# Kernel tuning notes

Hardware: AMD Instinct MI355X
Metric: run time of the kernel (lower is better)

Reference implementation:

```python
import jax, jax.numpy as jnp
import numpy as np

D_MODEL = 1024
N_HEADS = 16
D_HEAD = D_MODEL // N_HEADS


def setup_inputs() -> dict:
    key = jax.random.key(0)
    ks = jax.random.split(key, 9)
    s = 1.0 / np.sqrt(D_MODEL)
    inp = {
        'x': jax.random.normal(ks[0], (2, 2048, D_MODEL), dtype=jnp.float32),
        'wq': jax.random.uniform(ks[1], (D_MODEL, D_MODEL), jnp.float32, -s, s),
        'bq': jnp.zeros((D_MODEL,), jnp.float32),
        'wk': jax.random.uniform(ks[2], (D_MODEL, D_MODEL), jnp.float32, -s, s),
        'bk': jnp.zeros((D_MODEL,), jnp.float32),
        'wv': jax.random.uniform(ks[3], (D_MODEL, D_MODEL), jnp.float32, -s, s),
        'bv': jnp.zeros((D_MODEL,), jnp.float32),
        'wo': jax.random.uniform(ks[4], (D_MODEL, D_MODEL), jnp.float32, -s, s),
        'bo': jnp.zeros((D_MODEL,), jnp.float32),
    }
    return inp


def reference(x, wq, bq, wk, bk, wv, bv, wo, bo):
    B, S, D = x.shape
    H, Dh = N_HEADS, D_HEAD
    # projections (dropout is identity in eval mode)
    q = (x @ wq + bq).reshape(B, S, H, Dh).transpose(0, 2, 1, 3)  # [B,H,S,Dh]
    k = (x @ wk + bk).reshape(B, S, H, Dh).transpose(0, 2, 1, 3)
    v = (x @ wv + bv).reshape(B, S, H, Dh).transpose(0, 2, 1, 3)
    scores = jnp.einsum('bhqd,bhkd->bhqk', q, k) / jnp.sqrt(jnp.float32(Dh))
    causal = jnp.tril(jnp.ones((S, S), dtype=bool))  # [S,S]
    scores = jnp.where(causal[None, None], scores, jnp.float32(-jnp.inf))
    attn = jax.nn.softmax(scores, axis=-1)
    out = jnp.einsum('bhqk,bhkd->bhqd', attn, v)  # [B,H,S,Dh]
    out = out.transpose(0, 2, 1, 3).reshape(B, S, D)
    return out @ wo + bo
```

## Files before the change

kernel.cpp:

```cpp
#include <hip/hip_runtime.h>
#include <hip/hip_bf16.h>
#include <stdint.h>

#define NH 16
#define DH 64
#define BATCH 2
#define SEQ 2048
#define DMODEL 1024

typedef __attribute__((ext_vector_type(8))) short short8;
typedef __attribute__((ext_vector_type(4))) float f32x4;

#define MFMA16(a, b, c) __builtin_amdgcn_mfma_f32_16x16x32_bf16(a, b, c, 0, 0, 0)

__device__ inline unsigned short f2bf(float f) {
    union { float f; unsigned u; } v; v.f = f;
    unsigned r = v.u + 0x7fff + ((v.u >> 16) & 1);
    return (unsigned short)(r >> 16);
}

__device__ inline void gload_lds16(const unsigned short* g, unsigned short* l) {
    __builtin_amdgcn_global_load_lds((const __attribute__((address_space(1))) void*)g,
                                     (__attribute__((address_space(3))) void*)l, 16, 0, 0);
}

__device__ inline float dpp16_max(float v) {
    int t;
    t = __builtin_amdgcn_mov_dpp(__float_as_int(v), 0x121, 0xf, 0xf, false);
    v = fmaxf(v, __int_as_float(t));
    t = __builtin_amdgcn_mov_dpp(__float_as_int(v), 0x122, 0xf, 0xf, false);
    v = fmaxf(v, __int_as_float(t));
    t = __builtin_amdgcn_mov_dpp(__float_as_int(v), 0x124, 0xf, 0xf, false);
    v = fmaxf(v, __int_as_float(t));
    t = __builtin_amdgcn_mov_dpp(__float_as_int(v), 0x128, 0xf, 0xf, false);
    v = fmaxf(v, __int_as_float(t));
    return v;
}
__device__ inline float dpp16_sum(float v) {
    int t;
    t = __builtin_amdgcn_mov_dpp(__float_as_int(v), 0x121, 0xf, 0xf, false);
    v += __int_as_float(t);
    t = __builtin_amdgcn_mov_dpp(__float_as_int(v), 0x122, 0xf, 0xf, false);
    v += __int_as_float(t);
    t = __builtin_amdgcn_mov_dpp(__float_as_int(v), 0x124, 0xf, 0xf, false);
    v += __int_as_float(t);
    t = __builtin_amdgcn_mov_dpp(__float_as_int(v), 0x128, 0xf, 0xf, false);
    v += __int_as_float(t);
    return v;
}

__global__ void k_cvt(const float* __restrict__ in, unsigned short* __restrict__ out) {
    size_t i = ((size_t)blockIdx.x * 256 + threadIdx.x) * 8;
    f32x4 a = *(const f32x4*)(in + i);
    f32x4 b = *(const f32x4*)(in + i + 4);
    short8 o;
    o[0] = (short)f2bf(a[0]); o[1] = (short)f2bf(a[1]);
    o[2] = (short)f2bf(a[2]); o[3] = (short)f2bf(a[3]);
    o[4] = (short)f2bf(b[0]); o[5] = (short)f2bf(b[1]);
    o[6] = (short)f2bf(b[2]); o[7] = (short)f2bf(b[3]);
    *(short8*)(out + i) = o;
}

__global__ void k_transpose_w4(const float* __restrict__ wq, const float* __restrict__ wk,
                               const float* __restrict__ wv, const float* __restrict__ wo,
                               unsigned short* __restrict__ qkvT, unsigned short* __restrict__ oT) {
    __shared__ float tile[32][33];
    const int z = blockIdx.z;
    const float* w = (z == 0) ? wq : (z == 1) ? wk : (z == 2) ? wv : wo;
    unsigned short* out = (z == 3) ? oT : qkvT + (size_t)z * 1024 * 1024;
    int k0 = blockIdx.x * 32, n0 = blockIdx.y * 32;
    int tx = threadIdx.x, ty = threadIdx.y;
    #pragma unroll
    for (int j = 0; j < 32; j += 8)
        tile[ty + j][tx] = w[(size_t)(k0 + ty + j) * DMODEL + n0 + tx];
    __syncthreads();
    #pragma unroll
    for (int j = 0; j < 32; j += 8)
        out[(size_t)(n0 + ty + j) * DMODEL + k0 + tx] = f2bf(tile[tx][ty + j]);
}

__global__ __launch_bounds__(256) void k_transpose_v(const unsigned short* __restrict__ v,
                                                     unsigned short* __restrict__ vt) {
    __shared__ __align__(16) unsigned short tile[64][72];
    int bh = blockIdx.y, st = blockIdx.x;
    const unsigned short* src = v + ((size_t)bh * SEQ + st * 64) * DH;
    int r = threadIdx.x >> 2, c = (threadIdx.x & 3) * 16;
    *(short8*)&tile[r][c]     = *(const short8*)&src[r * DH + c];
    *(short8*)&tile[r][c + 8] = *(const short8*)&src[r * DH + c + 8];
    __syncthreads();
    int d = r, sb = c;
    short8 o0, o1;
    #pragma unroll
    for (int j = 0; j < 8; ++j) { o0[j] = (short)tile[sb + j][d]; o1[j] = (short)tile[sb + 8 + j][d]; }
    unsigned short* dst = vt + ((size_t)bh * DH + d) * SEQ + st * 64 + sb;
    *(short8*)dst = o0;
    *(short8*)(dst + 8) = o1;
}

#define GEMM_BODY(A_, Bt_)                                                              \
    __shared__ __align__(16) unsigned short As[128 * 32];                               \
    __shared__ __align__(16) unsigned short Bs[128 * 32];                               \
    const int tid = threadIdx.x;                                                        \
    const int lane = tid & 63, wave = tid >> 6;                                         \
    const int wr = wave >> 1, wc = wave & 1;                                            \
    const int nwgx = gridDim.x;                                                         \
    const int flat = blockIdx.y * nwgx + blockIdx.x;                                    \
    const int qq = (nwgx * gridDim.y) >> 3;                                             \
    const int newid = (flat & 7) * qq + (flat >> 3);                                    \
    const int row0 = (newid / nwgx) * 128, col0 = (newid % nwgx) * 128;                 \
    const int frow = lane & 15, fk = (lane >> 4) * 8;                                   \
    f32x4 acc[4][4] = {};                                                               \
    const int lr = tid >> 2;                                                            \
    const int lc = (tid & 3) * 8;                                                       \
    const unsigned short* ga0 = A_ + (size_t)(row0 + lr) * 1024 + lc;                   \
    const unsigned short* gb0 = Bt_ + (size_t)(col0 + lr) * 1024 + lc;                  \
    for (int kt = 0; kt < 1024; kt += 32) {                                             \
        gload_lds16(ga0 + kt, As + wave * 512);                                         \
        gload_lds16(ga0 + 64 * 1024 + kt, As + 2048 + wave * 512);                      \
        gload_lds16(gb0 + kt, Bs + wave * 512);                                         \
        gload_lds16(gb0 + 64 * 1024 + kt, Bs + 2048 + wave * 512);                      \
        __syncthreads();                                                                \
        short8 af[4], bf[4];                                                            \
        _Pragma("unroll")                                                               \
        for (int m = 0; m < 4; ++m)                                                     \
            af[m] = *(const short8*)&As[(wr * 64 + m * 16 + frow) * 32 + fk];           \
        _Pragma("unroll")                                                               \
        for (int n = 0; n < 4; ++n)                                                     \
            bf[n] = *(const short8*)&Bs[(wc * 64 + n * 16 + frow) * 32 + fk];           \
        _Pragma("unroll")                                                               \
        for (int m = 0; m < 4; ++m)                                                     \
            _Pragma("unroll")                                                           \
            for (int n = 0; n < 4; ++n)                                                 \
                acc[m][n] = MFMA16(af[m], bf[n], acc[m][n]);                            \
        __syncthreads();                                                                \
    }

__global__ __launch_bounds__(256) void k_gemm_qkv(
    const unsigned short* __restrict__ A, const unsigned short* __restrict__ Bt,
    const float* __restrict__ bq, const float* __restrict__ bk, const float* __restrict__ bv,
    unsigned short* __restrict__ qo, unsigned short* __restrict__ ko,
    unsigned short* __restrict__ vo)
{
    GEMM_BODY(A, Bt)
    const int p = col0 >> 10;
    const float* bias = (p == 0) ? bq : ((p == 1) ? bk : bv);
    unsigned short* dst = (p == 0) ? qo : ((p == 1) ? ko : vo);
    const float scl = (p == 0) ? 0.125f : 1.0f;
    #pragma unroll
    for (int m = 0; m < 4; ++m) {
        #pragma unroll
        for (int n = 0; n < 4; ++n) {
            int gcol = col0 + wc * 64 + n * 16 + frow;
            int hn = gcol & 1023;
            int h = hn >> 6, d = hn & 63;
            #pragma unroll
            for (int i = 0; i < 4; ++i) {
                int grow = row0 + wr * 64 + m * 16 + (lane >> 4) * 4 + i;
                int b = grow >> 11, s = grow & 2047;
                float v = (acc[m][n][i] + bias[hn]) * scl;
                dst[((size_t)(b * NH + h) * SEQ + s) * DH + d] = f2bf(v);
            }
        }
    }
}

__global__ __launch_bounds__(256) void k_gemm_out(
    const unsigned short* __restrict__ A, const unsigned short* __restrict__ Bt,
    const float* __restrict__ bo, float* __restrict__ out)
{
    GEMM_BODY(A, Bt)
    #pragma unroll
    for (int m = 0; m < 4; ++m) {
        #pragma unroll
        for (int n = 0; n < 4; ++n) {
            int gcol = col0 + wc * 64 + n * 16 + frow;
            #pragma unroll
            for (int i = 0; i < 4; ++i) {
                int grow = row0 + wr * 64 + m * 16 + (lane >> 4) * 4 + i;
                out[(size_t)grow * DMODEL + gcol] = acc[m][n][i] + bo[gcol];
            }
        }
    }
}

__global__ __launch_bounds__(256) void k_attn(
    const unsigned short* __restrict__ Q, const unsigned short* __restrict__ K,
    const unsigned short* __restrict__ VT, unsigned short* __restrict__ O)
{
    __shared__ __align__(16) unsigned short Ks[2][64 * 64];
    __shared__ __align__(16) unsigned short Vs[2][64 * 64];
    __shared__ __align__(16) unsigned short Ps[4][16 * 72];
    const int tid = threadIdx.x, lane = tid & 63, wave = tid >> 6;
    const int p = blockIdx.x;
    const int L = ((p & 7) << 6) | (p >> 3);
    const int bh = L >> 4, pr = L & 15;
    const unsigned short* Qb = Q + (size_t)bh * SEQ * DH;
    const unsigned short* Kb = K + (size_t)bh * SEQ * DH;
    const unsigned short* Vb = VT + (size_t)bh * SEQ * DH;
    const int frow = lane & 15, fk = (lane >> 4) * 8;
    const int srow = lane >> 3;
    const int scol = ((lane & 7) ^ srow) << 3;
    const int bb = bh >> 4, hh = bh & 15;

    for (int rep = 0; rep < 2; ++rep) {
        const int qt = rep ? pr : 31 - pr;
        const int q0 = qt * 64;
        short8 qf[2];
        #pragma unroll
        for (int t = 0; t < 2; ++t)
            qf[t] = *(const short8*)&Qb[(size_t)(q0 + wave * 16 + frow) * DH + t * 32 + fk];
        f32x4 oacc[4] = {};
        float mrow[4], lrow[4];
        #pragma unroll
        for (int i = 0; i < 4; ++i) { mrow[i] = -INFINITY; lrow[i] = 0.f; }

        auto stage = [&](int b, int kv0) {
            #pragma unroll
            for (int rd = 0; rd < 2; ++rd) {
                int row = rd * 32 + wave * 8 + srow;
                gload_lds16(Kb + (size_t)(kv0 + row) * DH + scol,
                            &Ks[b][(rd * 32 + wave * 8) * 64]);
                gload_lds16(Vb + (size_t)row * SEQ + kv0 + scol,
                            &Vs[b][(rd * 32 + wave * 8) * 64]);
            }
        };

        auto compute = [&](int cb_, bool diag) {
            const char* kbase = (const char*)&Ks[cb_][0];
            const char* vbase = (const char*)&Vs[cb_][0];
            const int sw = (frow & 7) << 4;
            f32x4 sc[4];
            __builtin_amdgcn_s_setprio(1);
            #pragma unroll
            for (int n = 0; n < 4; ++n) {
                f32x4 s = {0.f, 0.f, 0.f, 0.f};
                #pragma unroll
                for (int t = 0; t < 2; ++t) {
                    int cbt = (t * 32 + fk) * 2;
                    short8 kb = *(const short8*)(kbase + (n * 16 + frow) * 128 + (cbt ^ sw));
                    s = MFMA16(qf[t], kb, s);
                }
                sc[n] = s;
            }
            __builtin_amdgcn_s_setprio(0);
            if (diag) {
                #pragma unroll
                for (int n = 0; n < 4; ++n) {
                    int col = n * 16 + frow;
                    #pragma unroll
                    for (int i = 0; i < 4; ++i) {
                        int qrel = wave * 16 + (lane >> 4) * 4 + i;
                        if (col > qrel) sc[n][i] = -INFINITY;
                    }
                }
            }
            float mx[4];
            #pragma unroll
            for (int i = 0; i < 4; ++i)
                mx[i] = dpp16_max(fmaxf(fmaxf(sc[0][i], sc[1][i]), fmaxf(sc[2][i], sc[3][i])));
            float dm = fmaxf(fmaxf(mx[0] - mrow[0], mx[1] - mrow[1]),
                             fmaxf(mx[2] - mrow[2], mx[3] - mrow[3]));
            if (__any(dm > 8.f)) {
                #pragma unroll
                for (int i = 0; i < 4; ++i) {
                    float mnew = fmaxf(mrow[i], mx[i]);
                    float scl = __expf(mrow[i] - mnew);
                    mrow[i] = mnew;
                    lrow[i] *= scl;
                    #pragma unroll
                    for (int n = 0; n < 4; ++n) oacc[n][i] *= scl;
                }
            }
            #pragma unroll
            for (int i = 0; i < 4; ++i) {
                float rsum = 0.f;
                #pragma unroll
                for (int n = 0; n < 4; ++n) {
                    float pv = __expf(sc[n][i] - mrow[i]);
                    sc[n][i] = pv;
                    rsum += pv;
                }
                lrow[i] += rsum;
            }
            #pragma unroll
            for (int n = 0; n < 4; ++n)
                #pragma unroll
                for (int i = 0; i < 4; ++i)
                    Ps[wave][((lane >> 4) * 4 + i) * 72 + n * 16 + frow] = f2bf(sc[n][i]);
            asm volatile("s_waitcnt lgkmcnt(0)" ::: "memory");
            short8 pa[2];
            #pragma unroll
            for (int t = 0; t < 2; ++t)
                pa[t] = *(const short8*)&Ps[wave][frow * 72 + t * 32 + fk];
            __builtin_amdgcn_s_setprio(1);
            #pragma unroll
            for (int n = 0; n < 4; ++n)
                #pragma unroll
                for (int t = 0; t < 2; ++t) {
                    int cbt = (t * 32 + fk) * 2;
                    short8 vb2 = *(const short8*)(vbase + (n * 16 + frow) * 128 + (cbt ^ sw));
                    oacc[n] = MFMA16(pa[t], vb2, oacc[n]);
                }
            __builtin_amdgcn_s_setprio(0);
        };

        stage(0, 0);
        int cur = 0;
        for (int kt = 0; kt < qt; ++kt) {
            stage(cur ^ 1, (kt + 1) * 64);
            asm volatile("s_waitcnt vmcnt(4)" ::: "memory");
            __builtin_amdgcn_s_barrier();
            compute(cur, false);
            __builtin_amdgcn_s_barrier();
            cur ^= 1;
        }
        asm volatile("s_waitcnt vmcnt(0)" ::: "memory");
        __builtin_amdgcn_s_barrier();
        compute(cur, true);
        float lt[4];
        #pragma unroll
        for (int i = 0; i < 4; ++i) lt[i] = dpp16_sum(lrow[i]);
        #pragma unroll
        for (int n = 0; n < 4; ++n) {
            #pragma unroll
            for (int i = 0; i < 4; ++i) {
                int qrow = q0 + wave * 16 + (lane >> 4) * 4 + i;
                float v = oacc[n][i] / lt[i];
                O[((size_t)(bb * SEQ + qrow)) * DMODEL + hh * DH + n * 16 + frow] = f2bf(v);
            }
        }
        __builtin_amdgcn_s_barrier();
    }
}

extern "C" void kernel_launch(void* const* d_in, const int* in_sizes, int n_in,
                              void* d_out, int out_size, void* d_ws, size_t ws_size,
                              hipStream_t stream) {
    const float* x  = (const float*)d_in[0];
    const float* wq = (const float*)d_in[1];
    const float* bq = (const float*)d_in[2];
    const float* wk = (const float*)d_in[3];
    const float* bk = (const float*)d_in[4];
    const float* wv = (const float*)d_in[5];
    const float* bv = (const float*)d_in[6];
    const float* wo = (const float*)d_in[7];
    const float* bo = (const float*)d_in[8];
    float* out = (float*)d_out;

    char* w = (char*)d_ws;
    unsigned short* xb    = (unsigned short*)(w);
    unsigned short* vT    = (unsigned short*)(w);
    unsigned short* wqkvT = (unsigned short*)(w + 8388608);
    unsigned short* woT   = (unsigned short*)(w + 14680064);
    unsigned short* qarr  = (unsigned short*)(w + 16777216);
    unsigned short* karr  = (unsigned short*)(w + 25165824);
    unsigned short* varr  = (unsigned short*)(w + 33554432);
    unsigned short* attnb = (unsigned short*)(w + 41943040);

    k_cvt<<<2048, 256, 0, stream>>>(x, xb);
    k_transpose_w4<<<dim3(32, 32, 4), dim3(32, 8), 0, stream>>>(wq, wk, wv, wo, wqkvT, woT);
    k_gemm_qkv<<<dim3(24, 32), 256, 0, stream>>>(xb, wqkvT, bq, bk, bv, qarr, karr, varr);
    k_transpose_v<<<dim3(32, 32), 256, 0, stream>>>(varr, vT);
    k_attn<<<dim3(512), 256, 0, stream>>>(qarr, karr, vT, attnb);
    k_gemm_out<<<dim3(8, 32), 256, 0, stream>>>(attnb, woT, bo, out);
}
```

Measured before the change: 207.5 us.

## Use 128-row query tiles with 8 waves sharing K/V stages in attention

The attention kernel now runs 512 threads per block. Each block handles one 128-row query tile, instead of two 64-row tiles processed one after the other. All 8 waves share each staged 64-row K/V tile, which halves the global-to-LDS traffic per query row, and each wave skips tiles that lie fully above its causal diagonal. The block-to-(batch,head,tile) mapping is changed to pair long and short tiles across neighbouring blocks for load balance. In exchange, waves near the top of a tile idle on the later K/V tiles, and 512-thread blocks can reduce scheduling flexibility.

```diff
diff --git a/kernel.cpp b/kernel.cpp
--- a/kernel.cpp
+++ b/kernel.cpp
@@ -183,17 +183,22 @@
     }
 }
 
-__global__ __launch_bounds__(256) void k_attn(
+__global__ __launch_bounds__(512) void k_attn(
     const unsigned short* __restrict__ Q, const unsigned short* __restrict__ K,
     const unsigned short* __restrict__ VT, unsigned short* __restrict__ O)
 {
     __shared__ __align__(16) unsigned short Ks[2][64 * 64];
     __shared__ __align__(16) unsigned short Vs[2][64 * 64];
-    __shared__ __align__(16) unsigned short Ps[4][16 * 72];
+    __shared__ __align__(16) unsigned short Ps[8][16 * 72];
     const int tid = threadIdx.x, lane = tid & 63, wave = tid >> 6;
     const int p = blockIdx.x;
-    const int L = ((p & 7) << 6) | (p >> 3);
-    const int bh = L >> 4, pr = L & 15;
+    const int x = p & 7, j = p >> 3;
+    const int hi = j >> 5, mid = (j >> 4) & 1, lo = j & 15;
+    const int qt = hi ? (15 - lo) : lo;
+    const int bh = x * 4 + hi * 2 + mid;
+    const int q0 = qt * 128;
+    const int q0abs = q0 + wave * 16;
+    const int nt = 2 * qt + 2;
     const unsigned short* Qb = Q + (size_t)bh * SEQ * DH;
     const unsigned short* Kb = K + (size_t)bh * SEQ * DH;
     const unsigned short* Vb = VT + (size_t)bh * SEQ * DH;
@@ -202,134 +207,127 @@
     const int scol = ((lane & 7) ^ srow) << 3;
     const int bb = bh >> 4, hh = bh & 15;
 
-    for (int rep = 0; rep < 2; ++rep) {
-        const int qt = rep ? pr : 31 - pr;
-        const int q0 = qt * 64;
-        short8 qf[2];
-        #pragma unroll
-        for (int t = 0; t < 2; ++t)
-            qf[t] = *(const short8*)&Qb[(size_t)(q0 + wave * 16 + frow) * DH + t * 32 + fk];
-        f32x4 oacc[4] = {};
-        float mrow[4], lrow[4];
-        #pragma unroll
-        for (int i = 0; i < 4; ++i) { mrow[i] = -INFINITY; lrow[i] = 0.f; }
-
-        auto stage = [&](int b, int kv0) {
-            #pragma unroll
-            for (int rd = 0; rd < 2; ++rd) {
-                int row = rd * 32 + wave * 8 + srow;
-                gload_lds16(Kb + (size_t)(kv0 + row) * DH + scol,
-                            &Ks[b][(rd * 32 + wave * 8) * 64]);
-                gload_lds16(Vb + (size_t)row * SEQ + kv0 + scol,
-                            &Vs[b][(rd * 32 + wave * 8) * 64]);
-            }
-        };
-
-        auto compute = [&](int cb_, bool diag) {
-            const char* kbase = (const char*)&Ks[cb_][0];
-            const char* vbase = (const char*)&Vs[cb_][0];
-            const int sw = (frow & 7) << 4;
-            f32x4 sc[4];
-            __builtin_amdgcn_s_setprio(1);
+    short8 qf[2];
+    #pragma unroll
+    for (int t = 0; t < 2; ++t)
+        qf[t] = *(const short8*)&Qb[(size_t)(q0abs + frow) * DH + t * 32 + fk];
+    f32x4 oacc[4] = {};
+    float mrow[4], lrow[4];
+    #pragma unroll
+    for (int i = 0; i < 4; ++i) { mrow[i] = -INFINITY; lrow[i] = 0.f; }
+
+    auto stage = [&](int b, int kv0) {
+        gload_lds16(Kb + (size_t)(kv0 + wave * 8 + srow) * DH + scol, &Ks[b][wave * 8 * 64]);
+        gload_lds16(Vb + (size_t)(wave * 8 + srow) * SEQ + kv0 + scol, &Vs[b][wave * 8 * 64]);
+    };
+
+    auto compute = [&](int cb_, int rb) {
+        const char* kbase = (const char*)&Ks[cb_][0];
+        const char* vbase = (const char*)&Vs[cb_][0];
+        const int sw = (frow & 7) << 4;
+        f32x4 sc[4];
+        __builtin_amdgcn_s_setprio(1);
+        #pragma unroll
+        for (int n = 0; n < 4; ++n) {
+            f32x4 s = {0.f, 0.f, 0.f, 0.f};
+            #pragma unroll
+            for (int t = 0; t < 2; ++t) {
+                int cbt = (t * 32 + fk) * 2;
+                short8 kb = *(const short8*)(kbase + (n * 16 + frow) * 128 + (cbt ^ sw));
+                s = MFMA16(qf[t], kb, s);
+            }
+            sc[n] = s;
+        }
+        __builtin_amdgcn_s_setprio(0);
+        if (rb < 63) {
             #pragma unroll
             for (int n = 0; n < 4; ++n) {
-                f32x4 s = {0.f, 0.f, 0.f, 0.f};
-                #pragma unroll
-                for (int t = 0; t < 2; ++t) {
-                    int cbt = (t * 32 + fk) * 2;
-                    short8 kb = *(const short8*)(kbase + (n * 16 + frow) * 128 + (cbt ^ sw));
-                    s = MFMA16(qf[t], kb, s);
-                }
-                sc[n] = s;
-            }
-            __builtin_amdgcn_s_setprio(0);
-            if (diag) {
-                #pragma unroll
-                for (int n = 0; n < 4; ++n) {
-                    int col = n * 16 + frow;
-                    #pragma unroll
-                    for (int i = 0; i < 4; ++i) {
-                        int qrel = wave * 16 + (lane >> 4) * 4 + i;
-                        if (col > qrel) sc[n][i] = -INFINITY;
-                    }
-                }
-            }
-            float mx[4];
-            #pragma unroll
-            for (int i = 0; i < 4; ++i)
-                mx[i] = dpp16_max(fmaxf(fmaxf(sc[0][i], sc[1][i]), fmaxf(sc[2][i], sc[3][i])));
-            float dm = fmaxf(fmaxf(mx[0] - mrow[0], mx[1] - mrow[1]),
-                             fmaxf(mx[2] - mrow[2], mx[3] - mrow[3]));
-            if (__any(dm > 8.f)) {
+                int colr = n * 16 + frow;
                 #pragma unroll
                 for (int i = 0; i < 4; ++i) {
-                    float mnew = fmaxf(mrow[i], mx[i]);
-                    float scl = __expf(mrow[i] - mnew);
-                    mrow[i] = mnew;
-                    lrow[i] *= scl;
-                    #pragma unroll
-                    for (int n = 0; n < 4; ++n) oacc[n][i] *= scl;
+                    int qrel = rb + (lane >> 4) * 4 + i;
+                    if (colr > qrel) sc[n][i] = -INFINITY;
                 }
             }
+        }
+        float mx[4];
+        #pragma unroll
+        for (int i = 0; i < 4; ++i)
+            mx[i] = dpp16_max(fmaxf(fmaxf(sc[0][i], sc[1][i]), fmaxf(sc[2][i], sc[3][i])));
+        float dm = fmaxf(fmaxf(mx[0] - mrow[0], mx[1] - mrow[1]),
+                         fmaxf(mx[2] - mrow[2], mx[3] - mrow[3]));
+        if (__any(dm > 8.f)) {
             #pragma unroll
             for (int i = 0; i < 4; ++i) {
-                float rsum = 0.f;
+                float mnew = fmaxf(mrow[i], mx[i]);
+                float scl = __expf(mrow[i] - mnew);
+                mrow[i] = mnew;
+                lrow[i] *= scl;
                 #pragma unroll
-                for (int n = 0; n < 4; ++n) {
-                    float pv = __expf(sc[n][i] - mrow[i]);
-                    sc[n][i] = pv;
-                    rsum += pv;
-                }
-                lrow[i] += rsum;
-            }
-            #pragma unroll
-            for (int n = 0; n < 4; ++n)
-                #pragma unroll
-                for (int i = 0; i < 4; ++i)
-                    Ps[wave][((lane >> 4) * 4 + i) * 72 + n * 16 + frow] = f2bf(sc[n][i]);
-            asm volatile("s_waitcnt lgkmcnt(0)" ::: "memory");
-            short8 pa[2];
-            #pragma unroll
-            for (int t = 0; t < 2; ++t)
-                pa[t] = *(const short8*)&Ps[wave][frow * 72 + t * 32 + fk];
-            __builtin_amdgcn_s_setprio(1);
-            #pragma unroll
-            for (int n = 0; n < 4; ++n)
-                #pragma unroll
-                for (int t = 0; t < 2; ++t) {
-                    int cbt = (t * 32 + fk) * 2;
-                    short8 vb2 = *(const short8*)(vbase + (n * 16 + frow) * 128 + (cbt ^ sw));
-                    oacc[n] = MFMA16(pa[t], vb2, oacc[n]);
-                }
-            __builtin_amdgcn_s_setprio(0);
-        };
-
-        stage(0, 0);
-        int cur = 0;
-        for (int kt = 0; kt < qt; ++kt) {
-            stage(cur ^ 1, (kt + 1) * 64);
-            asm volatile("s_waitcnt vmcnt(4)" ::: "memory");
-            __builtin_amdgcn_s_barrier();
-            compute(cur, false);
-            __builtin_amdgcn_s_barrier();
-            cur ^= 1;
-        }
-        asm volatile("s_waitcnt vmcnt(0)" ::: "memory");
+                for (int n = 0; n < 4; ++n) oacc[n][i] *= scl;
+            }
+        }
+        #pragma unroll
+        for (int i = 0; i < 4; ++i) {
+            float rsum = 0.f;
+            #pragma unroll
+            for (int n = 0; n < 4; ++n) {
+                float pv = __expf(sc[n][i] - mrow[i]);
+                sc[n][i] = pv;
+                rsum += pv;
+            }
+            lrow[i] += rsum;
+        }
+        #pragma unroll
+        for (int n = 0; n < 4; ++n)
+            #pragma unroll
+            for (int i = 0; i < 4; ++i)
+                Ps[wave][((lane >> 4) * 4 + i) * 72 + n * 16 + frow] = f2bf(sc[n][i]);
+        asm volatile("s_waitcnt lgkmcnt(0)" ::: "memory");
+        short8 pa[2];
+        #pragma unroll
+        for (int t = 0; t < 2; ++t)
+            pa[t] = *(const short8*)&Ps[wave][frow * 72 + t * 32 + fk];
+        __builtin_amdgcn_s_setprio(1);
+        #pragma unroll
+        for (int n = 0; n < 4; ++n)
+            #pragma unroll
+            for (int t = 0; t < 2; ++t) {
+                int cbt = (t * 32 + fk) * 2;
+                short8 vb2 = *(const short8*)(vbase + (n * 16 + frow) * 128 + (cbt ^ sw));
+                oacc[n] = MFMA16(pa[t], vb2, oacc[n]);
+            }
+        __builtin_amdgcn_s_setprio(0);
+    };
+
+    stage(0, 0);
+    int cur = 0;
+    for (int kt = 0; kt < nt - 1; ++kt) {
+        stage(cur ^ 1, (kt + 1) * 64);
+        asm volatile("s_waitcnt vmcnt(2)" ::: "memory");
         __builtin_amdgcn_s_barrier();
-        compute(cur, true);
-        float lt[4];
-        #pragma unroll
-        for (int i = 0; i < 4; ++i) lt[i] = dpp16_sum(lrow[i]);
-        #pragma unroll
-        for (int n = 0; n < 4; ++n) {
-            #pragma unroll
-            for (int i = 0; i < 4; ++i) {
-                int qrow = q0 + wave * 16 + (lane >> 4) * 4 + i;
-                float v = oacc[n][i] / lt[i];
-                O[((size_t)(bb * SEQ + qrow)) * DMODEL + hh * DH + n * 16 + frow] = f2bf(v);
-            }
-        }
+        int rb = q0abs - kt * 64;
+        if (rb >= -15) compute(cur, rb);
         __builtin_amdgcn_s_barrier();
+        cur ^= 1;
+    }
+    asm volatile("s_waitcnt vmcnt(0)" ::: "memory");
+    __builtin_amdgcn_s_barrier();
+    {
+        int rb = q0abs - (nt - 1) * 64;
+        if (rb >= -15) compute(cur, rb);
+    }
+    float lt[4];
+    #pragma unroll
+    for (int i = 0; i < 4; ++i) lt[i] = dpp16_sum(lrow[i]);
+    #pragma unroll
+    for (int n = 0; n < 4; ++n) {
+        #pragma unroll
+        for (int i = 0; i < 4; ++i) {
+            int qrow = q0abs + (lane >> 4) * 4 + i;
+            float v = oacc[n][i] / lt[i];
+            O[((size_t)(bb * SEQ + qrow)) * DMODEL + hh * DH + n * 16 + frow] = f2bf(v);
+        }
     }
 }
 
@@ -361,6 +359,6 @@
     k_transpose_w4<<<dim3(32, 32, 4), dim3(32, 8), 0, stream>>>(wq, wk, wv, wo, wqkvT, woT);
     k_gemm_qkv<<<dim3(24, 32), 256, 0, stream>>>(xb, wqkvT, bq, bk, bv, qarr, karr, varr);
     k_transpose_v<<<dim3(32, 32), 256, 0, stream>>>(varr, vT);
-    k_attn<<<dim3(512), 256, 0, stream>>>(qarr, karr, vT, attnb);
+    k_attn<<<dim3(512), 512, 0, stream>>>(qarr, karr, vT, attnb);
     k_gemm_out<<<dim3(8, 32), 256, 0, stream>>>(attnb, woT, bo, out);
 }
```

Result: no change. 208.2 us (+0.3%).
